# Kernel optimization log

Hardware: AMD Instinct MI355X
Metric: run time of the kernel (lower is better)

The kernel has to match this reference:

```python
import jax, jax.numpy as jnp
import numpy as np

H_SP, W_SP = 8, 8
NUM_HEADS = 6
SHARED = 96
DIM_Q, DIM_KV = 96, 192
WIN = H_SP * W_SP  # 64 tokens per window


def _rel_index():
    # Swin-style relative position index, static numpy computation
    coords = np.stack(np.meshgrid(np.arange(H_SP), np.arange(W_SP), indexing='ij'))
    cf = coords.reshape(2, -1)                      # [2, 64]
    rel = cf[:, :, None] - cf[:, None, :]           # [2, 64, 64]
    rel = rel.transpose(1, 2, 0).astype(np.int64)   # [64, 64, 2]
    rel[..., 0] += H_SP - 1
    rel[..., 1] += W_SP - 1
    rel[..., 0] *= 2 * W_SP - 1
    return rel.sum(-1)                              # [64, 64], values in [0, 225)

REL_IDX = jnp.asarray(_rel_index())


def setup_inputs() -> dict:
    key = jax.random.key(0)
    ks = jax.random.split(key, 12)
    B, H, W = 4, 256, 256
    f32 = jnp.float32
    std = 0.02
    return {
        'x_q':  jax.random.normal(ks[0], (B, DIM_Q, H, W), f32),
        'x_kv': jax.random.normal(ks[1], (B, DIM_KV, H, W), f32),
        'Wq': jax.random.normal(ks[2], (DIM_Q, SHARED), f32) * std,
        'bq': jnp.zeros((SHARED,), f32),
        'Wk': jax.random.normal(ks[3], (DIM_KV, SHARED), f32) * std,
        'bk': jnp.zeros((SHARED,), f32),
        'Wv': jax.random.normal(ks[4], (DIM_KV, SHARED), f32) * std,
        'bv': jnp.zeros((SHARED,), f32),
        'bias_table': jax.random.normal(ks[5], ((2 * H_SP - 1) * (2 * W_SP - 1), NUM_HEADS), f32) * std,
        'Wo': jax.random.normal(ks[6], (SHARED, DIM_Q), f32) * std,
        'bo': jnp.zeros((DIM_Q,), f32),
    }


def reference(x_q, x_kv, Wq, bq, Wk, bk, Wv, bv, bias_table, Wo, bo):
    B, Cq, H, W = x_q.shape
    nH, nW = H // H_SP, W // W_SP  # H, W divisible by window -> pad is a no-op
    hd = SHARED // NUM_HEADS
    scale = hd ** -0.5

    def to_windows(img):
        C = img.shape[1]
        x = img.reshape(B, C, nH, H_SP, nW, W_SP)
        return x.transpose(0, 2, 4, 3, 5, 1).reshape(-1, WIN, C)

    qw = to_windows(x_q)    # [nWin, 64, Cq]
    kvw = to_windows(x_kv)  # [nWin, 64, Ckv]

    def heads(x):
        return x.reshape(-1, WIN, NUM_HEADS, hd).transpose(0, 2, 1, 3)  # [nWin, h, 64, hd]

    q = heads(qw @ Wq + bq)
    k = heads(kvw @ Wk + bk)
    v = heads(kvw @ Wv + bv)

    attn = jnp.einsum('whqd,whkd->whqk', q, k) * scale  # [nWin, h, 64, 64]
    rel_bias = bias_table[REL_IDX].transpose(2, 0, 1)   # [h, 64, 64]
    attn = jax.nn.softmax(attn + rel_bias[None], axis=-1)

    out = jnp.einsum('whqk,whkd->whqd', attn, v)        # [nWin, h, 64, hd]
    out = out.transpose(0, 2, 1, 3).reshape(-1, WIN, SHARED)
    out = out @ Wo + bo                                 # [nWin, 64, Cq]

    # windows2img
    out = out.reshape(B, nH, nW, H_SP, W_SP, Cq)
    out = out.transpose(0, 1, 3, 2, 4, 5).reshape(B, H, W, Cq)
    return out.transpose(0, 3, 1, 2)  # [B, Cq, H, W]
```

## Files before the change

### kernel.cpp

```cpp
#include <hip/hip_runtime.h>

typedef short short8 __attribute__((ext_vector_type(8)));
typedef float f32x4 __attribute__((ext_vector_type(4)));
typedef unsigned short ushort;

#define MFMA(a, b, c) __builtin_amdgcn_mfma_f32_16x16x32_bf16(a, b, c, 0, 0, 0)

#define WS_WQT 0
#define WS_WKT 9216
#define WS_WVT 27648
#define WS_WOT 46080
#define WS_BIAS 55296
#define WS_TOTAL 56646

#define STR_A 104
#define U_A    0
#define U_VT   6656
#define STR_VT 72
#define U_PS   13568
#define U_BIAS 18176
#define U_TOTAL 19526

#define LOG2E 1.44269504f

#define DPP_F(v, ctrl) __int_as_float(__builtin_amdgcn_update_dpp(0, __float_as_int(v), ctrl, 0xF, 0xF, true))

__device__ __forceinline__ ushort f2bf(float x) {
    unsigned u = __float_as_uint(x);
    u = (u + 0x7FFFu + ((u >> 16) & 1u)) >> 16;
    return (ushort)u;
}
__device__ __forceinline__ float bf2f(ushort u) {
    return __uint_as_float(((unsigned)u) << 16);
}

__global__ void prep_weights(const float* __restrict__ Wq, const float* __restrict__ Wk,
                             const float* __restrict__ Wv, const float* __restrict__ Wo,
                             const float* __restrict__ btab, ushort* __restrict__ ws) {
    int idx = blockIdx.x * 256 + threadIdx.x;
    if (idx < WS_WKT) {
        int f = idx >> 9, w = idx & 511, lane = w >> 3, j = w & 7;
        int nt = f / 3, kt = f % 3;
        int n = nt * 16 + (lane & 15), k = kt * 32 + (lane >> 4) * 8 + j;
        ws[idx] = f2bf(Wq[k * 96 + n]);
    } else if (idx < WS_WVT) {
        int t = idx - WS_WKT;
        int f = t >> 9, w = t & 511, lane = w >> 3, j = w & 7;
        int kt6 = f / 6, nt = f % 6;
        int n = nt * 16 + (lane & 15), k = kt6 * 32 + (lane >> 4) * 8 + j;
        ws[idx] = f2bf(Wk[k * 96 + n]);
    } else if (idx < WS_WOT) {
        int t = idx - WS_WVT;
        int f = t >> 9, w = t & 511, lane = w >> 3, j = w & 7;
        int kt6 = f / 6, nt = f % 6;
        int n = nt * 16 + (lane & 15), k = kt6 * 32 + (lane >> 4) * 8 + j;
        ws[idx] = f2bf(Wv[k * 96 + n]);
    } else if (idx < WS_BIAS) {
        int t = idx - WS_WOT;
        int f = t >> 9, w = t & 511, lane = w >> 3, j = w & 7;
        int nt = f / 3, kt = f % 3;
        int n = nt * 16 + (lane & 15), k = kt * 32 + (lane >> 4) * 8 + j;
        ws[idx] = f2bf(Wo[k * 96 + n]);
    } else if (idx < WS_TOTAL) {
        ws[idx] = f2bf(btab[idx - WS_BIAS] * LOG2E);
    }
}

__device__ __forceinline__ void softmax16(f32x4 (&s)[4], float (&pr)[4][4]) {
    #pragma unroll
    for (int r = 0; r < 4; ++r) {
        float m = fmaxf(fmaxf(s[0][r], s[1][r]), fmaxf(s[2][r], s[3][r]));
        m = fmaxf(m, DPP_F(m, 0xB1));
        m = fmaxf(m, DPP_F(m, 0x4E));
        m = fmaxf(m, DPP_F(m, 0x124));
        m = fmaxf(m, DPP_F(m, 0x128));
        float l = 0.f;
        #pragma unroll
        for (int nt = 0; nt < 4; ++nt) { pr[nt][r] = exp2f(s[nt][r] - m); l += pr[nt][r]; }
        l += DPP_F(l, 0xB1); l += DPP_F(l, 0x4E);
        l += DPP_F(l, 0x124); l += DPP_F(l, 0x128);
        float inv = __builtin_amdgcn_rcpf(l);
        #pragma unroll
        for (int nt = 0; nt < 4; ++nt) pr[nt][r] *= inv;
    }
}

__global__ __launch_bounds__(256, 4) void swin_attn(
    const float* __restrict__ xq, const float* __restrict__ xkv,
    const float* __restrict__ bq, const float* __restrict__ bk,
    const float* __restrict__ bv, const float* __restrict__ bo,
    const ushort* __restrict__ ws, float* __restrict__ out)
{
    __shared__ __align__(16) ushort smem[U_TOTAL + 8];
    const int tid = threadIdx.x;
    const int wave = tid >> 6, lane = tid & 63;
    const int l15 = lane & 15, quad = lane >> 4;
    int wid = ((blockIdx.x & 7) << 9) | (blockIdx.x >> 3);
    const int b = wid >> 10;
    const int wh = (wid >> 5) & 31, ww = wid & 31;
    const int h0 = wh * 8, w0 = ww * 8;
    const int mt = wave;

    ushort* A     = smem + U_A;
    ushort* vt    = smem + U_VT;
    ushort* ps    = smem + U_PS + wave * 1152;
    ushort* biasl = smem + U_BIAS;

    float bqr[6], bkr[6], bvr[6];
    #pragma unroll
    for (int h = 0; h < 6; ++h) {
        bqr[h] = bq[h * 16 + l15]; bkr[h] = bk[h * 16 + l15]; bvr[h] = bv[h * 16 + l15];
    }

    int pc[3], pi[3];
    #pragma unroll
    for (int t = 0; t < 3; ++t) { int p = tid + t * 256; pc[t] = p % 96; pi[t] = p / 96; }

    const float* xqb = xq + (size_t)b * 96 * 65536;
    float4 pf[3][2];
    #pragma unroll
    for (int t = 0; t < 3; ++t) {
        const float* g = xqb + (size_t)pc[t] * 65536 + (h0 + pi[t]) * 256 + w0;
        pf[t][0] = *(const float4*)g; pf[t][1] = *(const float4*)(g + 4);
    }
    for (int i = tid; i < 1350; i += 256) biasl[i] = ws[WS_BIAS + i];

    #pragma unroll
    for (int t = 0; t < 3; ++t) {
        int base = (pi[t] * 8) * STR_A + pc[t];
        A[base]             = f2bf(pf[t][0].x); A[base + STR_A]     = f2bf(pf[t][0].y);
        A[base + 2 * STR_A] = f2bf(pf[t][0].z); A[base + 3 * STR_A] = f2bf(pf[t][0].w);
        A[base + 4 * STR_A] = f2bf(pf[t][1].x); A[base + 5 * STR_A] = f2bf(pf[t][1].y);
        A[base + 6 * STR_A] = f2bf(pf[t][1].z); A[base + 7 * STR_A] = f2bf(pf[t][1].w);
    }
    __syncthreads();

    const float* xkvb = xkv + (size_t)b * 192 * 65536;
    float4 pg[3][2];
    #pragma unroll
    for (int t = 0; t < 3; ++t) {
        const float* g = xkvb + (size_t)pc[t] * 65536 + (h0 + pi[t]) * 256 + w0;
        pg[t][0] = *(const float4*)g; pg[t][1] = *(const float4*)(g + 4);
    }

    const int arow = (mt * 16 + l15) * STR_A + quad * 8;
    short8 a0 = *(const short8*)(A + arow);
    short8 a1 = *(const short8*)(A + arow + 32);
    short8 a2 = *(const short8*)(A + arow + 64);
    unsigned qpk[12];
    {
        short8 wq0 = *(const short8*)(ws + WS_WQT + ((0) * 64 + lane) * 8);
        short8 wq1 = *(const short8*)(ws + WS_WQT + ((1) * 64 + lane) * 8);
        short8 wq2 = *(const short8*)(ws + WS_WQT + ((2) * 64 + lane) * 8);
        #pragma unroll
        for (int h = 0; h < 6; ++h) {
            short8 c0 = wq0, c1 = wq1, c2 = wq2;
            if (h < 5) {
                wq0 = *(const short8*)(ws + WS_WQT + (((h + 1) * 3 + 0) * 64 + lane) * 8);
                wq1 = *(const short8*)(ws + WS_WQT + (((h + 1) * 3 + 1) * 64 + lane) * 8);
                wq2 = *(const short8*)(ws + WS_WQT + (((h + 1) * 3 + 2) * 64 + lane) * 8);
            }
            f32x4 qa = {bqr[h], bqr[h], bqr[h], bqr[h]};
            qa = MFMA(a0, c0, qa);
            qa = MFMA(a1, c1, qa);
            qa = MFMA(a2, c2, qa);
            const float qs = 0.25f * LOG2E;
            qpk[h * 2]     = (unsigned)f2bf(qa[0] * qs) | ((unsigned)f2bf(qa[1] * qs) << 16);
            qpk[h * 2 + 1] = (unsigned)f2bf(qa[2] * qs) | ((unsigned)f2bf(qa[3] * qs) << 16);
        }
    }
    __syncthreads();

    #pragma unroll
    for (int t = 0; t < 3; ++t) {
        int base = (pi[t] * 8) * STR_A + pc[t];
        A[base]             = f2bf(pg[t][0].x); A[base + STR_A]     = f2bf(pg[t][0].y);
        A[base + 2 * STR_A] = f2bf(pg[t][0].z); A[base + 3 * STR_A] = f2bf(pg[t][0].w);
        A[base + 4 * STR_A] = f2bf(pg[t][1].x); A[base + 5 * STR_A] = f2bf(pg[t][1].y);
        A[base + 6 * STR_A] = f2bf(pg[t][1].z); A[base + 7 * STR_A] = f2bf(pg[t][1].w);
    }
    __syncthreads();

    f32x4 accK[6], accV[6];
    #pragma unroll
    for (int n = 0; n < 6; ++n) {
        accK[n] = {bkr[n], bkr[n], bkr[n], bkr[n]};
        accV[n] = {bvr[n], bvr[n], bvr[n], bvr[n]};
    }
    #pragma unroll
    for (int kt = 0; kt < 3; ++kt) {
        short8 a = *(const short8*)(A + arow + kt * 32);
        short8 wkf[6], wvf[6];
        #pragma unroll
        for (int nt = 0; nt < 6; ++nt)
            wkf[nt] = *(const short8*)(ws + WS_WKT + (((kt * 6) + nt) * 64 + lane) * 8);
        #pragma unroll
        for (int nt = 0; nt < 6; ++nt)
            wvf[nt] = *(const short8*)(ws + WS_WVT + (((kt * 6) + nt) * 64 + lane) * 8);
        #pragma unroll
        for (int nt = 0; nt < 6; ++nt) accK[nt] = MFMA(a, wkf[nt], accK[nt]);
        #pragma unroll
        for (int nt = 0; nt < 6; ++nt) accV[nt] = MFMA(a, wvf[nt], accV[nt]);
    }
    #pragma unroll
    for (int t = 0; t < 3; ++t) {
        const float* g = xkvb + (size_t)(96 + pc[t]) * 65536 + (h0 + pi[t]) * 256 + w0;
        pf[t][0] = *(const float4*)g; pf[t][1] = *(const float4*)(g + 4);
    }
    __syncthreads();

    #pragma unroll
    for (int t = 0; t < 3; ++t) {
        int base = (pi[t] * 8) * STR_A + pc[t];
        A[base]             = f2bf(pf[t][0].x); A[base + STR_A]     = f2bf(pf[t][0].y);
        A[base + 2 * STR_A] = f2bf(pf[t][0].z); A[base + 3 * STR_A] = f2bf(pf[t][0].w);
        A[base + 4 * STR_A] = f2bf(pf[t][1].x); A[base + 5 * STR_A] = f2bf(pf[t][1].y);
        A[base + 6 * STR_A] = f2bf(pf[t][1].z); A[base + 7 * STR_A] = f2bf(pf[t][1].w);
    }
    __syncthreads();

    #pragma unroll
    for (int kt = 0; kt < 3; ++kt) {
        short8 a = *(const short8*)(A + arow + kt * 32);
        short8 wkf[6], wvf[6];
        #pragma unroll
        for (int nt = 0; nt < 6; ++nt)
            wkf[nt] = *(const short8*)(ws + WS_WKT + ((((3 + kt) * 6) + nt) * 64 + lane) * 8);
        #pragma unroll
        for (int nt = 0; nt < 6; ++nt)
            wvf[nt] = *(const short8*)(ws + WS_WVT + ((((3 + kt) * 6) + nt) * 64 + lane) * 8);
        #pragma unroll
        for (int nt = 0; nt < 6; ++nt) accK[nt] = MFMA(a, wkf[nt], accK[nt]);
        #pragma unroll
        for (int nt = 0; nt < 6; ++nt) accV[nt] = MFMA(a, wvf[nt], accV[nt]);
    }
    #pragma unroll
    for (int nt = 0; nt < 6; ++nt) {
        ushort* dk = A + (mt * 16 + quad * 4) * STR_A + nt * 16 + l15;
        ushort* dv = vt + nt * (16 * STR_VT) + l15 * STR_VT + (mt * 16 + quad * 4);
        #pragma unroll
        for (int r = 0; r < 4; ++r) {
            dk[r * STR_A] = f2bf(accK[nt][r]);
            dv[r]         = f2bf(accV[nt][r]);
        }
    }
    __syncthreads();

    const int qtok0 = mt * 16 + quad * 4;
    unsigned bidxp[4][2];
    #pragma unroll
    for (int nt = 0; nt < 4; ++nt) {
        int kt2 = nt * 16 + l15, i2 = kt2 >> 3, j2 = kt2 & 7;
        unsigned v[4];
        #pragma unroll
        for (int r = 0; r < 4; ++r) {
            int qt = qtok0 + r, i1 = qt >> 3, j1 = qt & 7;
            v[r] = (unsigned)(((i1 - i2 + 7) * 15 + (j1 - j2 + 7)) * 6);
        }
        bidxp[nt][0] = v[0] | (v[1] << 16);
        bidxp[nt][1] = v[2] | (v[3] << 16);
    }

    f32x4 accO[6];
    short8 zero8 = {};
    #pragma unroll
    for (int hp = 0; hp < 3; ++hp) {
        const int hA = hp * 2, hB = hA + 1;
        asm volatile("" ::: "memory");
        unsigned wloA = qpk[hA * 2], whiA = qpk[hA * 2 + 1];
        unsigned wloB = qpk[hB * 2], whiB = qpk[hB * 2 + 1];
        ps[(quad * 4 + 0) * 24 + l15] = (ushort)wloA;
        ps[(quad * 4 + 1) * 24 + l15] = (ushort)(wloA >> 16);
        ps[(quad * 4 + 2) * 24 + l15] = (ushort)whiA;
        ps[(quad * 4 + 3) * 24 + l15] = (ushort)(whiA >> 16);
        ps[384 + (quad * 4 + 0) * 24 + l15] = (ushort)wloB;
        ps[384 + (quad * 4 + 1) * 24 + l15] = (ushort)(wloB >> 16);
        ps[384 + (quad * 4 + 2) * 24 + l15] = (ushort)whiB;
        ps[384 + (quad * 4 + 3) * 24 + l15] = (ushort)(whiB >> 16);
        short8 aqA = zero8, aqB = zero8;
        short8 kfA[4] = {zero8, zero8, zero8, zero8};
        short8 kfB[4] = {zero8, zero8, zero8, zero8};
        if (quad < 2) {
            aqA = *(const short8*)(ps + l15 * 24 + quad * 8);
            aqB = *(const short8*)(ps + 384 + l15 * 24 + quad * 8);
            #pragma unroll
            for (int nt = 0; nt < 4; ++nt) {
                kfA[nt] = *(const short8*)(A + (nt * 16 + l15) * STR_A + hA * 16 + quad * 8);
                kfB[nt] = *(const short8*)(A + (nt * 16 + l15) * STR_A + hB * 16 + quad * 8);
            }
        }
        f32x4 sA[4], sB[4];
        #pragma unroll
        for (int nt = 0; nt < 4; ++nt) {
            unsigned i01 = bidxp[nt][0], i23 = bidxp[nt][1];
            f32x4 c;
            c[0] = bf2f(biasl[(i01 & 0xFFFFu) + hA]); c[1] = bf2f(biasl[(i01 >> 16) + hA]);
            c[2] = bf2f(biasl[(i23 & 0xFFFFu) + hA]); c[3] = bf2f(biasl[(i23 >> 16) + hA]);
            sA[nt] = MFMA(aqA, kfA[nt], c);
        }
        #pragma unroll
        for (int nt = 0; nt < 4; ++nt) {
            unsigned i01 = bidxp[nt][0], i23 = bidxp[nt][1];
            f32x4 c;
            c[0] = bf2f(biasl[(i01 & 0xFFFFu) + hB]); c[1] = bf2f(biasl[(i01 >> 16) + hB]);
            c[2] = bf2f(biasl[(i23 & 0xFFFFu) + hB]); c[3] = bf2f(biasl[(i23 >> 16) + hB]);
            sB[nt] = MFMA(aqB, kfB[nt], c);
        }
        float prA[4][4], prB[4][4];
        softmax16(sA, prA);
        softmax16(sB, prB);
        asm volatile("" ::: "memory");
        #pragma unroll
        for (int nt = 0; nt < 4; ++nt)
            #pragma unroll
            for (int r = 0; r < 4; ++r)
                ps[(quad * 4 + r) * 72 + nt * 16 + l15] = f2bf(prA[nt][r]);
        f32x4 oA = {};
        #pragma unroll
        for (int k2 = 0; k2 < 2; ++k2) {
            short8 ap  = *(const short8*)(ps + l15 * 72 + k2 * 32 + quad * 8);
            short8 bv8 = *(const short8*)(vt + hA * (16 * STR_VT) + l15 * STR_VT + k2 * 32 + quad * 8);
            oA = MFMA(ap, bv8, oA);
        }
        asm volatile("" ::: "memory");
        #pragma unroll
        for (int nt = 0; nt < 4; ++nt)
            #pragma unroll
            for (int r = 0; r < 4; ++r)
                ps[(quad * 4 + r) * 72 + nt * 16 + l15] = f2bf(prB[nt][r]);
        f32x4 oB = {};
        #pragma unroll
        for (int k2 = 0; k2 < 2; ++k2) {
            short8 ap  = *(const short8*)(ps + l15 * 72 + k2 * 32 + quad * 8);
            short8 bv8 = *(const short8*)(vt + hB * (16 * STR_VT) + l15 * STR_VT + k2 * 32 + quad * 8);
            oB = MFMA(ap, bv8, oB);
        }
        accO[hA] = oA; accO[hB] = oB;
    }
    __syncthreads();

    float bor_[6];
    #pragma unroll
    for (int h = 0; h < 6; ++h) bor_[h] = bo[h * 16 + l15];
    ushort* obuf = A;
    #pragma unroll
    for (int h = 0; h < 6; ++h)
        #pragma unroll
        for (int r = 0; r < 4; ++r)
            obuf[(mt * 16 + quad * 4 + r) * STR_A + h * 16 + l15] = f2bf(accO[h][r]);

    {
        int t0 = mt * 16 + quad * 4;
        int i = t0 >> 3, j0 = t0 & 7;
        short8 oa0 = *(const short8*)(obuf + arow);
        short8 oa1 = *(const short8*)(obuf + arow + 32);
        short8 oa2 = *(const short8*)(obuf + arow + 64);
        short8 wo0 = *(const short8*)(ws + WS_WOT + ((0) * 64 + lane) * 8);
        short8 wo1 = *(const short8*)(ws + WS_WOT + ((1) * 64 + lane) * 8);
        short8 wo2 = *(const short8*)(ws + WS_WOT + ((2) * 64 + lane) * 8);
        #pragma unroll
        for (int nt = 0; nt < 6; ++nt) {
            short8 c0 = wo0, c1 = wo1, c2 = wo2;
            if (nt < 5) {
                wo0 = *(const short8*)(ws + WS_WOT + (((nt + 1) * 3 + 0) * 64 + lane) * 8);
                wo1 = *(const short8*)(ws + WS_WOT + (((nt + 1) * 3 + 1) * 64 + lane) * 8);
                wo2 = *(const short8*)(ws + WS_WOT + (((nt + 1) * 3 + 2) * 64 + lane) * 8);
            }
            f32x4 acc = {bor_[nt], bor_[nt], bor_[nt], bor_[nt]};
            acc = MFMA(oa0, c0, acc);
            acc = MFMA(oa1, c1, acc);
            acc = MFMA(oa2, c2, acc);
            int cout = nt * 16 + l15;
            float4 v4 = make_float4(acc[0], acc[1], acc[2], acc[3]);
            float* dst = out + (size_t)(b * 96 + cout) * 65536 + (h0 + i) * 256 + w0 + j0;
            *(float4*)dst = v4;
        }
    }
}

extern "C" void kernel_launch(void* const* d_in, const int* in_sizes, int n_in,
                              void* d_out, int out_size, void* d_ws, size_t ws_size,
                              hipStream_t stream) {
    const float* xq   = (const float*)d_in[0];
    const float* xkv  = (const float*)d_in[1];
    const float* Wq   = (const float*)d_in[2];
    const float* bq   = (const float*)d_in[3];
    const float* Wk   = (const float*)d_in[4];
    const float* bk   = (const float*)d_in[5];
    const float* Wv   = (const float*)d_in[6];
    const float* bv   = (const float*)d_in[7];
    const float* btab = (const float*)d_in[8];
    const float* Wo   = (const float*)d_in[9];
    const float* bo   = (const float*)d_in[10];
    ushort* ws = (ushort*)d_ws;
    float* out = (float*)d_out;

    hipLaunchKernelGGL(prep_weights, dim3((WS_TOTAL + 255) / 256), dim3(256), 0, stream,
                       Wq, Wk, Wv, Wo, btab, ws);
    hipLaunchKernelGGL(swin_attn, dim3(4096), dim3(256), 0, stream,
                       xq, xkv, bq, bk, bv, bo, ws, out);
}
```

Before: 485.7 us.

## Transpose QK^T mapping, use bpermute for Q, prefetch K/V weights, pack bf16

Swaps MFMA operand order for the Q projection and QK^T so each lane holds a full key column per query, which turns softmax reductions into two cross-lane shuffles instead of DPP chains. Q fragments move between lanes with ds_bpermute instead of a shared-memory round trip. K/V weight fragments are software-prefetched one k-step ahead, with asm pins to force early issue. Conversions use v_cvt_pk_bf16_f32, and head-pair bias values are read with one 32-bit load. Occupancy hint drops from 4 to 3 waves per SIMD to make room for the extra live registers.

```diff
diff --git a/kernel.cpp b/kernel.cpp
--- a/kernel.cpp
+++ b/kernel.cpp
@@ -2,9 +2,15 @@
 
 typedef short short8 __attribute__((ext_vector_type(8)));
 typedef float f32x4 __attribute__((ext_vector_type(4)));
+typedef int int4v __attribute__((ext_vector_type(4)));
+typedef unsigned uint2v __attribute__((ext_vector_type(2)));
 typedef unsigned short ushort;
 
 #define MFMA(a, b, c) __builtin_amdgcn_mfma_f32_16x16x32_bf16(a, b, c, 0, 0, 0)
+
+#define PIN8(v8_) do { int4v _t; __builtin_memcpy(&_t, &(v8_), 16); \
+    asm volatile("" :: "v"(_t[0]), "v"(_t[1]), "v"(_t[2]), "v"(_t[3])); } while (0)
+#define PINF4(v4_) asm volatile("" :: "v"((v4_).x), "v"((v4_).y), "v"((v4_).z), "v"((v4_).w))
 
 #define WS_WQT 0
 #define WS_WKT 9216
@@ -23,15 +29,15 @@
 
 #define LOG2E 1.44269504f
 
-#define DPP_F(v, ctrl) __int_as_float(__builtin_amdgcn_update_dpp(0, __float_as_int(v), ctrl, 0xF, 0xF, true))
-
-__device__ __forceinline__ ushort f2bf(float x) {
-    unsigned u = __float_as_uint(x);
+__device__ __forceinline__ ushort f2bf(float v) {
+    unsigned u = __float_as_uint(v);
     u = (u + 0x7FFFu + ((u >> 16) & 1u)) >> 16;
     return (ushort)u;
 }
-__device__ __forceinline__ float bf2f(ushort u) {
-    return __uint_as_float(((unsigned)u) << 16);
+__device__ __forceinline__ unsigned cvtpk_bf16(float lo, float hi) {
+    unsigned r;
+    asm("v_cvt_pk_bf16_f32 %0, %1, %2" : "=v"(r) : "v"(lo), "v"(hi));
+    return r;
 }
 
 __global__ void prep_weights(const float* __restrict__ Wq, const float* __restrict__ Wk,
@@ -66,26 +72,7 @@
     }
 }
 
-__device__ __forceinline__ void softmax16(f32x4 (&s)[4], float (&pr)[4][4]) {
-    #pragma unroll
-    for (int r = 0; r < 4; ++r) {
-        float m = fmaxf(fmaxf(s[0][r], s[1][r]), fmaxf(s[2][r], s[3][r]));
-        m = fmaxf(m, DPP_F(m, 0xB1));
-        m = fmaxf(m, DPP_F(m, 0x4E));
-        m = fmaxf(m, DPP_F(m, 0x124));
-        m = fmaxf(m, DPP_F(m, 0x128));
-        float l = 0.f;
-        #pragma unroll
-        for (int nt = 0; nt < 4; ++nt) { pr[nt][r] = exp2f(s[nt][r] - m); l += pr[nt][r]; }
-        l += DPP_F(l, 0xB1); l += DPP_F(l, 0x4E);
-        l += DPP_F(l, 0x124); l += DPP_F(l, 0x128);
-        float inv = __builtin_amdgcn_rcpf(l);
-        #pragma unroll
-        for (int nt = 0; nt < 4; ++nt) pr[nt][r] *= inv;
-    }
-}
-
-__global__ __launch_bounds__(256, 4) void swin_attn(
+__global__ __launch_bounds__(256, 3) void swin_attn(
     const float* __restrict__ xq, const float* __restrict__ xkv,
     const float* __restrict__ bq, const float* __restrict__ bk,
     const float* __restrict__ bv, const float* __restrict__ bo,
@@ -106,11 +93,9 @@
     ushort* ps    = smem + U_PS + wave * 1152;
     ushort* biasl = smem + U_BIAS;
 
-    float bqr[6], bkr[6], bvr[6];
-    #pragma unroll
-    for (int h = 0; h < 6; ++h) {
-        bqr[h] = bq[h * 16 + l15]; bkr[h] = bk[h * 16 + l15]; bvr[h] = bv[h * 16 + l15];
-    }
+    float bkr[6], bvr[6];
+    #pragma unroll
+    for (int h = 0; h < 6; ++h) { bkr[h] = bk[h * 16 + l15]; bvr[h] = bv[h * 16 + l15]; }
 
     int pc[3], pi[3];
     #pragma unroll
@@ -141,7 +126,11 @@
     for (int t = 0; t < 3; ++t) {
         const float* g = xkvb + (size_t)pc[t] * 65536 + (h0 + pi[t]) * 256 + w0;
         pg[t][0] = *(const float4*)g; pg[t][1] = *(const float4*)(g + 4);
-    }
+        PINF4(pg[t][0]); PINF4(pg[t][1]);
+    }
+    float4 bqv[6];
+    #pragma unroll
+    for (int h = 0; h < 6; ++h) { bqv[h] = *(const float4*)(bq + h * 16 + quad * 4); PINF4(bqv[h]); }
 
     const int arow = (mt * 16 + l15) * STR_A + quad * 8;
     short8 a0 = *(const short8*)(A + arow);
@@ -149,9 +138,10 @@
     short8 a2 = *(const short8*)(A + arow + 64);
     unsigned qpk[12];
     {
-        short8 wq0 = *(const short8*)(ws + WS_WQT + ((0) * 64 + lane) * 8);
-        short8 wq1 = *(const short8*)(ws + WS_WQT + ((1) * 64 + lane) * 8);
-        short8 wq2 = *(const short8*)(ws + WS_WQT + ((2) * 64 + lane) * 8);
+        short8 wq0 = *(const short8*)(ws + WS_WQT + (0 * 64 + lane) * 8);
+        short8 wq1 = *(const short8*)(ws + WS_WQT + (1 * 64 + lane) * 8);
+        short8 wq2 = *(const short8*)(ws + WS_WQT + (2 * 64 + lane) * 8);
+        PIN8(wq0); PIN8(wq1); PIN8(wq2);
         #pragma unroll
         for (int h = 0; h < 6; ++h) {
             short8 c0 = wq0, c1 = wq1, c2 = wq2;
@@ -159,14 +149,15 @@
                 wq0 = *(const short8*)(ws + WS_WQT + (((h + 1) * 3 + 0) * 64 + lane) * 8);
                 wq1 = *(const short8*)(ws + WS_WQT + (((h + 1) * 3 + 1) * 64 + lane) * 8);
                 wq2 = *(const short8*)(ws + WS_WQT + (((h + 1) * 3 + 2) * 64 + lane) * 8);
-            }
-            f32x4 qa = {bqr[h], bqr[h], bqr[h], bqr[h]};
-            qa = MFMA(a0, c0, qa);
-            qa = MFMA(a1, c1, qa);
-            qa = MFMA(a2, c2, qa);
+                PIN8(wq0); PIN8(wq1); PIN8(wq2);
+            }
+            f32x4 qa = {bqv[h].x, bqv[h].y, bqv[h].z, bqv[h].w};
+            qa = MFMA(c0, a0, qa);
+            qa = MFMA(c1, a1, qa);
+            qa = MFMA(c2, a2, qa);
             const float qs = 0.25f * LOG2E;
-            qpk[h * 2]     = (unsigned)f2bf(qa[0] * qs) | ((unsigned)f2bf(qa[1] * qs) << 16);
-            qpk[h * 2 + 1] = (unsigned)f2bf(qa[2] * qs) | ((unsigned)f2bf(qa[3] * qs) << 16);
+            qpk[h * 2]     = cvtpk_bf16(qa[0] * qs, qa[1] * qs);
+            qpk[h * 2 + 1] = cvtpk_bf16(qa[2] * qs, qa[3] * qs);
         }
     }
     __syncthreads();
@@ -179,33 +170,50 @@
         A[base + 4 * STR_A] = f2bf(pg[t][1].x); A[base + 5 * STR_A] = f2bf(pg[t][1].y);
         A[base + 6 * STR_A] = f2bf(pg[t][1].z); A[base + 7 * STR_A] = f2bf(pg[t][1].w);
     }
-    __syncthreads();
-
     f32x4 accK[6], accV[6];
     #pragma unroll
     for (int n = 0; n < 6; ++n) {
         accK[n] = {bkr[n], bkr[n], bkr[n], bkr[n]};
         accV[n] = {bvr[n], bvr[n], bvr[n], bvr[n]};
     }
+    short8 wk[6], wv[6];
+    #pragma unroll
+    for (int nt = 0; nt < 6; ++nt) {
+        wk[nt] = *(const short8*)(ws + WS_WKT + (nt * 64 + lane) * 8); PIN8(wk[nt]);
+    }
+    #pragma unroll
+    for (int nt = 0; nt < 6; ++nt) {
+        wv[nt] = *(const short8*)(ws + WS_WVT + (nt * 64 + lane) * 8); PIN8(wv[nt]);
+    }
+    __syncthreads();
+
     #pragma unroll
     for (int kt = 0; kt < 3; ++kt) {
         short8 a = *(const short8*)(A + arow + kt * 32);
-        short8 wkf[6], wvf[6];
-        #pragma unroll
-        for (int nt = 0; nt < 6; ++nt)
-            wkf[nt] = *(const short8*)(ws + WS_WKT + (((kt * 6) + nt) * 64 + lane) * 8);
-        #pragma unroll
-        for (int nt = 0; nt < 6; ++nt)
-            wvf[nt] = *(const short8*)(ws + WS_WVT + (((kt * 6) + nt) * 64 + lane) * 8);
-        #pragma unroll
-        for (int nt = 0; nt < 6; ++nt) accK[nt] = MFMA(a, wkf[nt], accK[nt]);
-        #pragma unroll
-        for (int nt = 0; nt < 6; ++nt) accV[nt] = MFMA(a, wvf[nt], accV[nt]);
+        #pragma unroll
+        for (int nt = 0; nt < 6; ++nt) accK[nt] = MFMA(a, wk[nt], accK[nt]);
+        if (kt < 2) {
+            #pragma unroll
+            for (int nt = 0; nt < 6; ++nt) {
+                wk[nt] = *(const short8*)(ws + WS_WKT + ((((kt + 1) * 6) + nt) * 64 + lane) * 8);
+                PIN8(wk[nt]);
+            }
+        }
+        #pragma unroll
+        for (int nt = 0; nt < 6; ++nt) accV[nt] = MFMA(a, wv[nt], accV[nt]);
+        if (kt < 2) {
+            #pragma unroll
+            for (int nt = 0; nt < 6; ++nt) {
+                wv[nt] = *(const short8*)(ws + WS_WVT + ((((kt + 1) * 6) + nt) * 64 + lane) * 8);
+                PIN8(wv[nt]);
+            }
+        }
     }
     #pragma unroll
     for (int t = 0; t < 3; ++t) {
         const float* g = xkvb + (size_t)(96 + pc[t]) * 65536 + (h0 + pi[t]) * 256 + w0;
         pf[t][0] = *(const float4*)g; pf[t][1] = *(const float4*)(g + 4);
+        PINF4(pf[t][0]); PINF4(pf[t][1]);
     }
     __syncthreads();
 
@@ -217,22 +225,37 @@
         A[base + 4 * STR_A] = f2bf(pf[t][1].x); A[base + 5 * STR_A] = f2bf(pf[t][1].y);
         A[base + 6 * STR_A] = f2bf(pf[t][1].z); A[base + 7 * STR_A] = f2bf(pf[t][1].w);
     }
+    #pragma unroll
+    for (int nt = 0; nt < 6; ++nt) {
+        wk[nt] = *(const short8*)(ws + WS_WKT + (((3 * 6) + nt) * 64 + lane) * 8); PIN8(wk[nt]);
+    }
+    #pragma unroll
+    for (int nt = 0; nt < 6; ++nt) {
+        wv[nt] = *(const short8*)(ws + WS_WVT + (((3 * 6) + nt) * 64 + lane) * 8); PIN8(wv[nt]);
+    }
     __syncthreads();
 
     #pragma unroll
     for (int kt = 0; kt < 3; ++kt) {
         short8 a = *(const short8*)(A + arow + kt * 32);
-        short8 wkf[6], wvf[6];
-        #pragma unroll
-        for (int nt = 0; nt < 6; ++nt)
-            wkf[nt] = *(const short8*)(ws + WS_WKT + ((((3 + kt) * 6) + nt) * 64 + lane) * 8);
-        #pragma unroll
-        for (int nt = 0; nt < 6; ++nt)
-            wvf[nt] = *(const short8*)(ws + WS_WVT + ((((3 + kt) * 6) + nt) * 64 + lane) * 8);
-        #pragma unroll
-        for (int nt = 0; nt < 6; ++nt) accK[nt] = MFMA(a, wkf[nt], accK[nt]);
-        #pragma unroll
-        for (int nt = 0; nt < 6; ++nt) accV[nt] = MFMA(a, wvf[nt], accV[nt]);
+        #pragma unroll
+        for (int nt = 0; nt < 6; ++nt) accK[nt] = MFMA(a, wk[nt], accK[nt]);
+        if (kt < 2) {
+            #pragma unroll
+            for (int nt = 0; nt < 6; ++nt) {
+                wk[nt] = *(const short8*)(ws + WS_WKT + ((((4 + kt) * 6) + nt) * 64 + lane) * 8);
+                PIN8(wk[nt]);
+            }
+        }
+        #pragma unroll
+        for (int nt = 0; nt < 6; ++nt) accV[nt] = MFMA(a, wv[nt], accV[nt]);
+        if (kt < 2) {
+            #pragma unroll
+            for (int nt = 0; nt < 6; ++nt) {
+                wv[nt] = *(const short8*)(ws + WS_WVT + ((((4 + kt) * 6) + nt) * 64 + lane) * 8);
+                PIN8(wv[nt]);
+            }
+        }
     }
     #pragma unroll
     for (int nt = 0; nt < 6; ++nt) {
@@ -246,92 +269,133 @@
     }
     __syncthreads();
 
-    const int qtok0 = mt * 16 + quad * 4;
-    unsigned bidxp[4][2];
-    #pragma unroll
-    for (int nt = 0; nt < 4; ++nt) {
-        int kt2 = nt * 16 + l15, i2 = kt2 >> 3, j2 = kt2 & 7;
-        unsigned v[4];
+    const int qt = mt * 16 + l15;
+    const int i1 = qt >> 3, j1 = qt & 7;
+    int boff[4][4];
+    #pragma unroll
+    for (int nt = 0; nt < 4; ++nt)
         #pragma unroll
         for (int r = 0; r < 4; ++r) {
-            int qt = qtok0 + r, i1 = qt >> 3, j1 = qt & 7;
-            v[r] = (unsigned)(((i1 - i2 + 7) * 15 + (j1 - j2 + 7)) * 6);
-        }
-        bidxp[nt][0] = v[0] | (v[1] << 16);
-        bidxp[nt][1] = v[2] | (v[3] << 16);
-    }
+            int k2 = nt * 16 + quad * 4 + r, i2 = k2 >> 3, j2 = k2 & 7;
+            boff[nt][r] = ((i1 - i2 + 7) * 15 + (j1 - j2 + 7)) * 6;
+        }
+
+    const int bp0 = (l15 + (quad << 5)) << 2;
+    const int bp1 = bp0 + (16 << 2);
+    const int psrow = l15 * 72;
 
     f32x4 accO[6];
     short8 zero8 = {};
     #pragma unroll
     for (int hp = 0; hp < 3; ++hp) {
         const int hA = hp * 2, hB = hA + 1;
-        asm volatile("" ::: "memory");
-        unsigned wloA = qpk[hA * 2], whiA = qpk[hA * 2 + 1];
-        unsigned wloB = qpk[hB * 2], whiB = qpk[hB * 2 + 1];
-        ps[(quad * 4 + 0) * 24 + l15] = (ushort)wloA;
-        ps[(quad * 4 + 1) * 24 + l15] = (ushort)(wloA >> 16);
-        ps[(quad * 4 + 2) * 24 + l15] = (ushort)whiA;
-        ps[(quad * 4 + 3) * 24 + l15] = (ushort)(whiA >> 16);
-        ps[384 + (quad * 4 + 0) * 24 + l15] = (ushort)wloB;
-        ps[384 + (quad * 4 + 1) * 24 + l15] = (ushort)(wloB >> 16);
-        ps[384 + (quad * 4 + 2) * 24 + l15] = (ushort)whiB;
-        ps[384 + (quad * 4 + 3) * 24 + l15] = (ushort)(whiB >> 16);
-        short8 aqA = zero8, aqB = zero8;
-        short8 kfA[4] = {zero8, zero8, zero8, zero8};
-        short8 kfB[4] = {zero8, zero8, zero8, zero8};
+        int A0 = __builtin_amdgcn_ds_bpermute(bp0, (int)qpk[hA * 2]);
+        int A1 = __builtin_amdgcn_ds_bpermute(bp0, (int)qpk[hA * 2 + 1]);
+        int A2 = __builtin_amdgcn_ds_bpermute(bp1, (int)qpk[hA * 2]);
+        int A3 = __builtin_amdgcn_ds_bpermute(bp1, (int)qpk[hA * 2 + 1]);
+        int B0 = __builtin_amdgcn_ds_bpermute(bp0, (int)qpk[hB * 2]);
+        int B1 = __builtin_amdgcn_ds_bpermute(bp0, (int)qpk[hB * 2 + 1]);
+        int B2 = __builtin_amdgcn_ds_bpermute(bp1, (int)qpk[hB * 2]);
+        int B3 = __builtin_amdgcn_ds_bpermute(bp1, (int)qpk[hB * 2 + 1]);
+        union { int4v i; short8 s; } ua, ub;
+        ua.i = (int4v){A0, A1, A2, A3};
+        ub.i = (int4v){B0, B1, B2, B3};
+        short8 aqA = ua.s, aqB = ub.s;
+
+        short8 kfA[4], kfB[4];
+        #pragma unroll
+        for (int nt = 0; nt < 4; ++nt) { kfA[nt] = zero8; kfB[nt] = zero8; }
         if (quad < 2) {
-            aqA = *(const short8*)(ps + l15 * 24 + quad * 8);
-            aqB = *(const short8*)(ps + 384 + l15 * 24 + quad * 8);
             #pragma unroll
             for (int nt = 0; nt < 4; ++nt) {
                 kfA[nt] = *(const short8*)(A + (nt * 16 + l15) * STR_A + hA * 16 + quad * 8);
                 kfB[nt] = *(const short8*)(A + (nt * 16 + l15) * STR_A + hB * 16 + quad * 8);
             }
         }
+        unsigned bb[4][4];
+        #pragma unroll
+        for (int nt = 0; nt < 4; ++nt)
+            #pragma unroll
+            for (int r = 0; r < 4; ++r)
+                bb[nt][r] = *(const unsigned*)(biasl + boff[nt][r] + hA);
+
         f32x4 sA[4], sB[4];
         #pragma unroll
         for (int nt = 0; nt < 4; ++nt) {
-            unsigned i01 = bidxp[nt][0], i23 = bidxp[nt][1];
             f32x4 c;
-            c[0] = bf2f(biasl[(i01 & 0xFFFFu) + hA]); c[1] = bf2f(biasl[(i01 >> 16) + hA]);
-            c[2] = bf2f(biasl[(i23 & 0xFFFFu) + hA]); c[3] = bf2f(biasl[(i23 >> 16) + hA]);
-            sA[nt] = MFMA(aqA, kfA[nt], c);
+            c[0] = __uint_as_float(bb[nt][0] << 16); c[1] = __uint_as_float(bb[nt][1] << 16);
+            c[2] = __uint_as_float(bb[nt][2] << 16); c[3] = __uint_as_float(bb[nt][3] << 16);
+            sA[nt] = MFMA(kfA[nt], aqA, c);
         }
         #pragma unroll
         for (int nt = 0; nt < 4; ++nt) {
-            unsigned i01 = bidxp[nt][0], i23 = bidxp[nt][1];
             f32x4 c;
-            c[0] = bf2f(biasl[(i01 & 0xFFFFu) + hB]); c[1] = bf2f(biasl[(i01 >> 16) + hB]);
-            c[2] = bf2f(biasl[(i23 & 0xFFFFu) + hB]); c[3] = bf2f(biasl[(i23 >> 16) + hB]);
-            sB[nt] = MFMA(aqB, kfB[nt], c);
-        }
-        float prA[4][4], prB[4][4];
-        softmax16(sA, prA);
-        softmax16(sB, prB);
-        asm volatile("" ::: "memory");
+            c[0] = __uint_as_float(bb[nt][0] & 0xFFFF0000u); c[1] = __uint_as_float(bb[nt][1] & 0xFFFF0000u);
+            c[2] = __uint_as_float(bb[nt][2] & 0xFFFF0000u); c[3] = __uint_as_float(bb[nt][3] & 0xFFFF0000u);
+            sB[nt] = MFMA(kfB[nt], aqB, c);
+        }
+        float mA, mB, lA, lB;
+        {
+            float a_ = fmaxf(fmaxf(sA[0][0], sA[0][1]), fmaxf(sA[0][2], sA[0][3]));
+            float b_ = fmaxf(fmaxf(sA[1][0], sA[1][1]), fmaxf(sA[1][2], sA[1][3]));
+            float c_ = fmaxf(fmaxf(sA[2][0], sA[2][1]), fmaxf(sA[2][2], sA[2][3]));
+            float d_ = fmaxf(fmaxf(sA[3][0], sA[3][1]), fmaxf(sA[3][2], sA[3][3]));
+            mA = fmaxf(fmaxf(a_, b_), fmaxf(c_, d_));
+            float a2_ = fmaxf(fmaxf(sB[0][0], sB[0][1]), fmaxf(sB[0][2], sB[0][3]));
+            float b2_ = fmaxf(fmaxf(sB[1][0], sB[1][1]), fmaxf(sB[1][2], sB[1][3]));
+            float c2_ = fmaxf(fmaxf(sB[2][0], sB[2][1]), fmaxf(sB[2][2], sB[2][3]));
+            float d2_ = fmaxf(fmaxf(sB[3][0], sB[3][1]), fmaxf(sB[3][2], sB[3][3]));
+            mB = fmaxf(fmaxf(a2_, b2_), fmaxf(c2_, d2_));
+        }
+        mA = fmaxf(mA, __shfl_xor(mA, 16)); mA = fmaxf(mA, __shfl_xor(mA, 32));
+        mB = fmaxf(mB, __shfl_xor(mB, 16)); mB = fmaxf(mB, __shfl_xor(mB, 32));
         #pragma unroll
         for (int nt = 0; nt < 4; ++nt)
             #pragma unroll
-            for (int r = 0; r < 4; ++r)
-                ps[(quad * 4 + r) * 72 + nt * 16 + l15] = f2bf(prA[nt][r]);
+            for (int r = 0; r < 4; ++r) {
+                sA[nt][r] = exp2f(sA[nt][r] - mA);
+                sB[nt][r] = exp2f(sB[nt][r] - mB);
+            }
+        {
+            float a_ = (sA[0][0] + sA[0][1]) + (sA[0][2] + sA[0][3]);
+            float b_ = (sA[1][0] + sA[1][1]) + (sA[1][2] + sA[1][3]);
+            float c_ = (sA[2][0] + sA[2][1]) + (sA[2][2] + sA[2][3]);
+            float d_ = (sA[3][0] + sA[3][1]) + (sA[3][2] + sA[3][3]);
+            lA = (a_ + b_) + (c_ + d_);
+            float a2_ = (sB[0][0] + sB[0][1]) + (sB[0][2] + sB[0][3]);
+            float b2_ = (sB[1][0] + sB[1][1]) + (sB[1][2] + sB[1][3]);
+            float c2_ = (sB[2][0] + sB[2][1]) + (sB[2][2] + sB[2][3]);
+            float d2_ = (sB[3][0] + sB[3][1]) + (sB[3][2] + sB[3][3]);
+            lB = (a2_ + b2_) + (c2_ + d2_);
+        }
+        lA += __shfl_xor(lA, 16); lA += __shfl_xor(lA, 32);
+        lB += __shfl_xor(lB, 16); lB += __shfl_xor(lB, 32);
+        float invA = __builtin_amdgcn_rcpf(lA);
+        float invB = __builtin_amdgcn_rcpf(lB);
+
+        #pragma unroll
+        for (int nt = 0; nt < 4; ++nt) {
+            unsigned p0 = cvtpk_bf16(sA[nt][0] * invA, sA[nt][1] * invA);
+            unsigned p1 = cvtpk_bf16(sA[nt][2] * invA, sA[nt][3] * invA);
+            *(uint2v*)(ps + psrow + nt * 16 + quad * 4) = (uint2v){p0, p1};
+        }
         f32x4 oA = {};
         #pragma unroll
         for (int k2 = 0; k2 < 2; ++k2) {
-            short8 ap  = *(const short8*)(ps + l15 * 72 + k2 * 32 + quad * 8);
+            short8 ap  = *(const short8*)(ps + psrow + k2 * 32 + quad * 8);
             short8 bv8 = *(const short8*)(vt + hA * (16 * STR_VT) + l15 * STR_VT + k2 * 32 + quad * 8);
             oA = MFMA(ap, bv8, oA);
         }
-        asm volatile("" ::: "memory");
-        #pragma unroll
-        for (int nt = 0; nt < 4; ++nt)
-            #pragma unroll
-            for (int r = 0; r < 4; ++r)
-                ps[(quad * 4 + r) * 72 + nt * 16 + l15] = f2bf(prB[nt][r]);
+        #pragma unroll
+        for (int nt = 0; nt < 4; ++nt) {
+            unsigned p0 = cvtpk_bf16(sB[nt][0] * invB, sB[nt][1] * invB);
+            unsigned p1 = cvtpk_bf16(sB[nt][2] * invB, sB[nt][3] * invB);
+            *(uint2v*)(ps + psrow + nt * 16 + quad * 4) = (uint2v){p0, p1};
+        }
         f32x4 oB = {};
         #pragma unroll
         for (int k2 = 0; k2 < 2; ++k2) {
-            short8 ap  = *(const short8*)(ps + l15 * 72 + k2 * 32 + quad * 8);
+            short8 ap  = *(const short8*)(ps + psrow + k2 * 32 + quad * 8);
             short8 bv8 = *(const short8*)(vt + hB * (16 * STR_VT) + l15 * STR_VT + k2 * 32 + quad * 8);
             oB = MFMA(ap, bv8, oB);
         }
@@ -355,9 +419,10 @@
         short8 oa0 = *(const short8*)(obuf + arow);
         short8 oa1 = *(const short8*)(obuf + arow + 32);
         short8 oa2 = *(const short8*)(obuf + arow + 64);
-        short8 wo0 = *(const short8*)(ws + WS_WOT + ((0) * 64 + lane) * 8);
-        short8 wo1 = *(const short8*)(ws + WS_WOT + ((1) * 64 + lane) * 8);
-        short8 wo2 = *(const short8*)(ws + WS_WOT + ((2) * 64 + lane) * 8);
+        short8 wo0 = *(const short8*)(ws + WS_WOT + (0 * 64 + lane) * 8);
+        short8 wo1 = *(const short8*)(ws + WS_WOT + (1 * 64 + lane) * 8);
+        short8 wo2 = *(const short8*)(ws + WS_WOT + (2 * 64 + lane) * 8);
+        PIN8(wo0); PIN8(wo1); PIN8(wo2);
         #pragma unroll
         for (int nt = 0; nt < 6; ++nt) {
             short8 c0 = wo0, c1 = wo1, c2 = wo2;
@@ -365,6 +430,7 @@
                 wo0 = *(const short8*)(ws + WS_WOT + (((nt + 1) * 3 + 0) * 64 + lane) * 8);
                 wo1 = *(const short8*)(ws + WS_WOT + (((nt + 1) * 3 + 1) * 64 + lane) * 8);
                 wo2 = *(const short8*)(ws + WS_WOT + (((nt + 1) * 3 + 2) * 64 + lane) * 8);
+                PIN8(wo0); PIN8(wo1); PIN8(wo2);
             }
             f32x4 acc = {bor_[nt], bor_[nt], bor_[nt], bor_[nt]};
             acc = MFMA(oa0, c0, acc);
```

After: 554.4 us. 1.14x slower.

## Remap input staging per token, pack bf16 conversions, defer softmax normalization

Applied to the files above, without the earlier changes.

Each lane now loads one token across 24 channels, so the input tile is written to LDS as packed bf16 vectors with `v_cvt_pk_bf16_f32`. This replaces many scattered 16-bit stores. The first K/V input chunk is staged in the V-transpose region, which removes one barrier between the Q projection and the K/V projection. Softmax no longer subtracts the row max, and normalization moves after the PV MFMA as a per-row scale. Bias values for the two heads are fetched with a single 32-bit LDS load. Dropping the max subtraction risks overflow in exp2 if scores grow large, and the new global loads are 4-byte scalars instead of float4.

```diff
diff --git a/kernel.cpp b/kernel.cpp
--- a/kernel.cpp
+++ b/kernel.cpp
@@ -2,9 +2,11 @@
 
 typedef short short8 __attribute__((ext_vector_type(8)));
 typedef float f32x4 __attribute__((ext_vector_type(4)));
+typedef unsigned uint4v __attribute__((ext_vector_type(4)));
 typedef unsigned short ushort;
 
 #define MFMA(a, b, c) __builtin_amdgcn_mfma_f32_16x16x32_bf16(a, b, c, 0, 0, 0)
+#define DPP_F(v, ctrl) __int_as_float(__builtin_amdgcn_update_dpp(0, __float_as_int(v), ctrl, 0xF, 0xF, true))
 
 #define WS_WQT 0
 #define WS_WKT 9216
@@ -23,15 +25,15 @@
 
 #define LOG2E 1.44269504f
 
-#define DPP_F(v, ctrl) __int_as_float(__builtin_amdgcn_update_dpp(0, __float_as_int(v), ctrl, 0xF, 0xF, true))
-
-__device__ __forceinline__ ushort f2bf(float x) {
-    unsigned u = __float_as_uint(x);
+__device__ __forceinline__ ushort f2bf(float v) {
+    unsigned u = __float_as_uint(v);
     u = (u + 0x7FFFu + ((u >> 16) & 1u)) >> 16;
     return (ushort)u;
 }
-__device__ __forceinline__ float bf2f(ushort u) {
-    return __uint_as_float(((unsigned)u) << 16);
+__device__ __forceinline__ unsigned cvtpk_bf16(float lo, float hi) {
+    unsigned r;
+    asm("v_cvt_pk_bf16_f32 %0, %1, %2" : "=v"(r) : "v"(lo), "v"(hi));
+    return r;
 }
 
 __global__ void prep_weights(const float* __restrict__ Wq, const float* __restrict__ Wk,
@@ -66,25 +68,6 @@
     }
 }
 
-__device__ __forceinline__ void softmax16(f32x4 (&s)[4], float (&pr)[4][4]) {
-    #pragma unroll
-    for (int r = 0; r < 4; ++r) {
-        float m = fmaxf(fmaxf(s[0][r], s[1][r]), fmaxf(s[2][r], s[3][r]));
-        m = fmaxf(m, DPP_F(m, 0xB1));
-        m = fmaxf(m, DPP_F(m, 0x4E));
-        m = fmaxf(m, DPP_F(m, 0x124));
-        m = fmaxf(m, DPP_F(m, 0x128));
-        float l = 0.f;
-        #pragma unroll
-        for (int nt = 0; nt < 4; ++nt) { pr[nt][r] = exp2f(s[nt][r] - m); l += pr[nt][r]; }
-        l += DPP_F(l, 0xB1); l += DPP_F(l, 0x4E);
-        l += DPP_F(l, 0x124); l += DPP_F(l, 0x128);
-        float inv = __builtin_amdgcn_rcpf(l);
-        #pragma unroll
-        for (int nt = 0; nt < 4; ++nt) pr[nt][r] *= inv;
-    }
-}
-
 __global__ __launch_bounds__(256, 4) void swin_attn(
     const float* __restrict__ xq, const float* __restrict__ xkv,
     const float* __restrict__ bq, const float* __restrict__ bk,
@@ -102,7 +85,7 @@
     const int mt = wave;
 
     ushort* A     = smem + U_A;
-    ushort* vt    = smem + U_VT;
+    ushort* vtreg = smem + U_VT;
     ushort* ps    = smem + U_PS + wave * 1152;
     ushort* biasl = smem + U_BIAS;
 
@@ -112,72 +95,65 @@
         bqr[h] = bq[h * 16 + l15]; bkr[h] = bk[h * 16 + l15]; bvr[h] = bv[h * 16 + l15];
     }
 
-    int pc[3], pi[3];
-    #pragma unroll
-    for (int t = 0; t < 3; ++t) { int p = tid + t * 256; pc[t] = p % 96; pi[t] = p / 96; }
+    const int c0   = __builtin_amdgcn_readfirstlane(wave * 24);
+    const int toff = (h0 + (lane >> 3)) * 256 + w0 + (lane & 7);
+    const int wdst = lane * STR_A + c0;
+    const int arow = (mt * 16 + l15) * STR_A + quad * 8;
 
     const float* xqb = xq + (size_t)b * 96 * 65536;
-    float4 pf[3][2];
-    #pragma unroll
-    for (int t = 0; t < 3; ++t) {
-        const float* g = xqb + (size_t)pc[t] * 65536 + (h0 + pi[t]) * 256 + w0;
-        pf[t][0] = *(const float4*)g; pf[t][1] = *(const float4*)(g + 4);
-    }
+    float vq[24];
+    #pragma unroll
+    for (int j = 0; j < 24; ++j) vq[j] = xqb[(size_t)(c0 + j) * 65536 + toff];
     for (int i = tid; i < 1350; i += 256) biasl[i] = ws[WS_BIAS + i];
-
-    #pragma unroll
-    for (int t = 0; t < 3; ++t) {
-        int base = (pi[t] * 8) * STR_A + pc[t];
-        A[base]             = f2bf(pf[t][0].x); A[base + STR_A]     = f2bf(pf[t][0].y);
-        A[base + 2 * STR_A] = f2bf(pf[t][0].z); A[base + 3 * STR_A] = f2bf(pf[t][0].w);
-        A[base + 4 * STR_A] = f2bf(pf[t][1].x); A[base + 5 * STR_A] = f2bf(pf[t][1].y);
-        A[base + 6 * STR_A] = f2bf(pf[t][1].z); A[base + 7 * STR_A] = f2bf(pf[t][1].w);
+    {
+        unsigned u[12];
+        #pragma unroll
+        for (int j = 0; j < 12; ++j) u[j] = cvtpk_bf16(vq[2 * j], vq[2 * j + 1]);
+        uint4v* d = (uint4v*)(A + wdst);
+        d[0] = (uint4v){u[0], u[1], u[2], u[3]};
+        d[1] = (uint4v){u[4], u[5], u[6], u[7]};
+        d[2] = (uint4v){u[8], u[9], u[10], u[11]};
     }
     __syncthreads();
 
     const float* xkvb = xkv + (size_t)b * 192 * 65536;
-    float4 pg[3][2];
-    #pragma unroll
-    for (int t = 0; t < 3; ++t) {
-        const float* g = xkvb + (size_t)pc[t] * 65536 + (h0 + pi[t]) * 256 + w0;
-        pg[t][0] = *(const float4*)g; pg[t][1] = *(const float4*)(g + 4);
-    }
-
-    const int arow = (mt * 16 + l15) * STR_A + quad * 8;
+    float vk0[24];
+    #pragma unroll
+    for (int j = 0; j < 24; ++j) vk0[j] = xkvb[(size_t)(c0 + j) * 65536 + toff];
+
     short8 a0 = *(const short8*)(A + arow);
     short8 a1 = *(const short8*)(A + arow + 32);
     short8 a2 = *(const short8*)(A + arow + 64);
     unsigned qpk[12];
     {
-        short8 wq0 = *(const short8*)(ws + WS_WQT + ((0) * 64 + lane) * 8);
-        short8 wq1 = *(const short8*)(ws + WS_WQT + ((1) * 64 + lane) * 8);
-        short8 wq2 = *(const short8*)(ws + WS_WQT + ((2) * 64 + lane) * 8);
+        short8 wq0 = *(const short8*)(ws + WS_WQT + (0 * 64 + lane) * 8);
+        short8 wq1 = *(const short8*)(ws + WS_WQT + (1 * 64 + lane) * 8);
+        short8 wq2 = *(const short8*)(ws + WS_WQT + (2 * 64 + lane) * 8);
         #pragma unroll
         for (int h = 0; h < 6; ++h) {
-            short8 c0 = wq0, c1 = wq1, c2 = wq2;
+            short8 c0f = wq0, c1f = wq1, c2f = wq2;
             if (h < 5) {
                 wq0 = *(const short8*)(ws + WS_WQT + (((h + 1) * 3 + 0) * 64 + lane) * 8);
                 wq1 = *(const short8*)(ws + WS_WQT + (((h + 1) * 3 + 1) * 64 + lane) * 8);
                 wq2 = *(const short8*)(ws + WS_WQT + (((h + 1) * 3 + 2) * 64 + lane) * 8);
             }
             f32x4 qa = {bqr[h], bqr[h], bqr[h], bqr[h]};
-            qa = MFMA(a0, c0, qa);
-            qa = MFMA(a1, c1, qa);
-            qa = MFMA(a2, c2, qa);
+            qa = MFMA(a0, c0f, qa);
+            qa = MFMA(a1, c1f, qa);
+            qa = MFMA(a2, c2f, qa);
             const float qs = 0.25f * LOG2E;
-            qpk[h * 2]     = (unsigned)f2bf(qa[0] * qs) | ((unsigned)f2bf(qa[1] * qs) << 16);
-            qpk[h * 2 + 1] = (unsigned)f2bf(qa[2] * qs) | ((unsigned)f2bf(qa[3] * qs) << 16);
-        }
-    }
-    __syncthreads();
-
-    #pragma unroll
-    for (int t = 0; t < 3; ++t) {
-        int base = (pi[t] * 8) * STR_A + pc[t];
-        A[base]             = f2bf(pg[t][0].x); A[base + STR_A]     = f2bf(pg[t][0].y);
-        A[base + 2 * STR_A] = f2bf(pg[t][0].z); A[base + 3 * STR_A] = f2bf(pg[t][0].w);
-        A[base + 4 * STR_A] = f2bf(pg[t][1].x); A[base + 5 * STR_A] = f2bf(pg[t][1].y);
-        A[base + 6 * STR_A] = f2bf(pg[t][1].z); A[base + 7 * STR_A] = f2bf(pg[t][1].w);
+            qpk[h * 2]     = cvtpk_bf16(qa[0] * qs, qa[1] * qs);
+            qpk[h * 2 + 1] = cvtpk_bf16(qa[2] * qs, qa[3] * qs);
+        }
+    }
+    {
+        unsigned u[12];
+        #pragma unroll
+        for (int j = 0; j < 12; ++j) u[j] = cvtpk_bf16(vk0[2 * j], vk0[2 * j + 1]);
+        uint4v* d = (uint4v*)(vtreg + wdst);
+        d[0] = (uint4v){u[0], u[1], u[2], u[3]};
+        d[1] = (uint4v){u[4], u[5], u[6], u[7]};
+        d[2] = (uint4v){u[8], u[9], u[10], u[11]};
     }
     __syncthreads();
 
@@ -189,7 +165,7 @@
     }
     #pragma unroll
     for (int kt = 0; kt < 3; ++kt) {
-        short8 a = *(const short8*)(A + arow + kt * 32);
+        short8 a = *(const short8*)(vtreg + arow + kt * 32);
         short8 wkf[6], wvf[6];
         #pragma unroll
         for (int nt = 0; nt < 6; ++nt)
@@ -202,20 +178,17 @@
         #pragma unroll
         for (int nt = 0; nt < 6; ++nt) accV[nt] = MFMA(a, wvf[nt], accV[nt]);
     }
-    #pragma unroll
-    for (int t = 0; t < 3; ++t) {
-        const float* g = xkvb + (size_t)(96 + pc[t]) * 65536 + (h0 + pi[t]) * 256 + w0;
-        pf[t][0] = *(const float4*)g; pf[t][1] = *(const float4*)(g + 4);
-    }
-    __syncthreads();
-
-    #pragma unroll
-    for (int t = 0; t < 3; ++t) {
-        int base = (pi[t] * 8) * STR_A + pc[t];
-        A[base]             = f2bf(pf[t][0].x); A[base + STR_A]     = f2bf(pf[t][0].y);
-        A[base + 2 * STR_A] = f2bf(pf[t][0].z); A[base + 3 * STR_A] = f2bf(pf[t][0].w);
-        A[base + 4 * STR_A] = f2bf(pf[t][1].x); A[base + 5 * STR_A] = f2bf(pf[t][1].y);
-        A[base + 6 * STR_A] = f2bf(pf[t][1].z); A[base + 7 * STR_A] = f2bf(pf[t][1].w);
+    {
+        float vk1[24];
+        #pragma unroll
+        for (int j = 0; j < 24; ++j) vk1[j] = xkvb[(size_t)(96 + c0 + j) * 65536 + toff];
+        unsigned u[12];
+        #pragma unroll
+        for (int j = 0; j < 12; ++j) u[j] = cvtpk_bf16(vk1[2 * j], vk1[2 * j + 1]);
+        uint4v* d = (uint4v*)(A + wdst);
+        d[0] = (uint4v){u[0], u[1], u[2], u[3]};
+        d[1] = (uint4v){u[4], u[5], u[6], u[7]};
+        d[2] = (uint4v){u[8], u[9], u[10], u[11]};
     }
     __syncthreads();
 
@@ -237,7 +210,7 @@
     #pragma unroll
     for (int nt = 0; nt < 6; ++nt) {
         ushort* dk = A + (mt * 16 + quad * 4) * STR_A + nt * 16 + l15;
-        ushort* dv = vt + nt * (16 * STR_VT) + l15 * STR_VT + (mt * 16 + quad * 4);
+        ushort* dv = vtreg + nt * (16 * STR_VT) + l15 * STR_VT + (mt * 16 + quad * 4);
         #pragma unroll
         for (int r = 0; r < 4; ++r) {
             dk[r * STR_A] = f2bf(accK[nt][r]);
@@ -289,26 +262,46 @@
                 kfB[nt] = *(const short8*)(A + (nt * 16 + l15) * STR_A + hB * 16 + quad * 8);
             }
         }
-        f32x4 sA[4], sB[4];
+        unsigned bb[4][4];
         #pragma unroll
         for (int nt = 0; nt < 4; ++nt) {
             unsigned i01 = bidxp[nt][0], i23 = bidxp[nt][1];
+            bb[nt][0] = *(const unsigned*)(biasl + (i01 & 0xFFFFu) + hA);
+            bb[nt][1] = *(const unsigned*)(biasl + (i01 >> 16) + hA);
+            bb[nt][2] = *(const unsigned*)(biasl + (i23 & 0xFFFFu) + hA);
+            bb[nt][3] = *(const unsigned*)(biasl + (i23 >> 16) + hA);
+        }
+        f32x4 sA[4], sB[4];
+        #pragma unroll
+        for (int nt = 0; nt < 4; ++nt) {
             f32x4 c;
-            c[0] = bf2f(biasl[(i01 & 0xFFFFu) + hA]); c[1] = bf2f(biasl[(i01 >> 16) + hA]);
-            c[2] = bf2f(biasl[(i23 & 0xFFFFu) + hA]); c[3] = bf2f(biasl[(i23 >> 16) + hA]);
+            c[0] = __uint_as_float(bb[nt][0] << 16); c[1] = __uint_as_float(bb[nt][1] << 16);
+            c[2] = __uint_as_float(bb[nt][2] << 16); c[3] = __uint_as_float(bb[nt][3] << 16);
             sA[nt] = MFMA(aqA, kfA[nt], c);
         }
         #pragma unroll
         for (int nt = 0; nt < 4; ++nt) {
-            unsigned i01 = bidxp[nt][0], i23 = bidxp[nt][1];
             f32x4 c;
-            c[0] = bf2f(biasl[(i01 & 0xFFFFu) + hB]); c[1] = bf2f(biasl[(i01 >> 16) + hB]);
-            c[2] = bf2f(biasl[(i23 & 0xFFFFu) + hB]); c[3] = bf2f(biasl[(i23 >> 16) + hB]);
+            c[0] = __uint_as_float(bb[nt][0] & 0xFFFF0000u); c[1] = __uint_as_float(bb[nt][1] & 0xFFFF0000u);
+            c[2] = __uint_as_float(bb[nt][2] & 0xFFFF0000u); c[3] = __uint_as_float(bb[nt][3] & 0xFFFF0000u);
             sB[nt] = MFMA(aqB, kfB[nt], c);
         }
-        float prA[4][4], prB[4][4];
-        softmax16(sA, prA);
-        softmax16(sB, prB);
+        float prA[4][4], prB[4][4], invA4[4], invB4[4];
+        #pragma unroll
+        for (int r = 0; r < 4; ++r) {
+            float lA = 0.f, lB = 0.f;
+            #pragma unroll
+            for (int nt = 0; nt < 4; ++nt) {
+                prA[nt][r] = exp2f(sA[nt][r]); lA += prA[nt][r];
+                prB[nt][r] = exp2f(sB[nt][r]); lB += prB[nt][r];
+            }
+            lA += DPP_F(lA, 0xB1);  lB += DPP_F(lB, 0xB1);
+            lA += DPP_F(lA, 0x4E);  lB += DPP_F(lB, 0x4E);
+            lA += DPP_F(lA, 0x124); lB += DPP_F(lB, 0x124);
+            lA += DPP_F(lA, 0x128); lB += DPP_F(lB, 0x128);
+            invA4[r] = __builtin_amdgcn_rcpf(lA);
+            invB4[r] = __builtin_amdgcn_rcpf(lB);
+        }
         asm volatile("" ::: "memory");
         #pragma unroll
         for (int nt = 0; nt < 4; ++nt)
@@ -319,9 +312,11 @@
         #pragma unroll
         for (int k2 = 0; k2 < 2; ++k2) {
             short8 ap  = *(const short8*)(ps + l15 * 72 + k2 * 32 + quad * 8);
-            short8 bv8 = *(const short8*)(vt + hA * (16 * STR_VT) + l15 * STR_VT + k2 * 32 + quad * 8);
+            short8 bv8 = *(const short8*)(vtreg + hA * (16 * STR_VT) + l15 * STR_VT + k2 * 32 + quad * 8);
             oA = MFMA(ap, bv8, oA);
         }
+        #pragma unroll
+        for (int r = 0; r < 4; ++r) oA[r] *= invA4[r];
         asm volatile("" ::: "memory");
         #pragma unroll
         for (int nt = 0; nt < 4; ++nt)
@@ -332,9 +327,11 @@
         #pragma unroll
         for (int k2 = 0; k2 < 2; ++k2) {
             short8 ap  = *(const short8*)(ps + l15 * 72 + k2 * 32 + quad * 8);
-            short8 bv8 = *(const short8*)(vt + hB * (16 * STR_VT) + l15 * STR_VT + k2 * 32 + quad * 8);
+            short8 bv8 = *(const short8*)(vtreg + hB * (16 * STR_VT) + l15 * STR_VT + k2 * 32 + quad * 8);
             oB = MFMA(ap, bv8, oB);
         }
+        #pragma unroll
+        for (int r = 0; r < 4; ++r) oB[r] *= invB4[r];
         accO[hA] = oA; accO[hB] = oB;
     }
     __syncthreads();
@@ -355,21 +352,21 @@
         short8 oa0 = *(const short8*)(obuf + arow);
         short8 oa1 = *(const short8*)(obuf + arow + 32);
         short8 oa2 = *(const short8*)(obuf + arow + 64);
-        short8 wo0 = *(const short8*)(ws + WS_WOT + ((0) * 64 + lane) * 8);
-        short8 wo1 = *(const short8*)(ws + WS_WOT + ((1) * 64 + lane) * 8);
-        short8 wo2 = *(const short8*)(ws + WS_WOT + ((2) * 64 + lane) * 8);
+        short8 wo0 = *(const short8*)(ws + WS_WOT + (0 * 64 + lane) * 8);
+        short8 wo1 = *(const short8*)(ws + WS_WOT + (1 * 64 + lane) * 8);
+        short8 wo2 = *(const short8*)(ws + WS_WOT + (2 * 64 + lane) * 8);
         #pragma unroll
         for (int nt = 0; nt < 6; ++nt) {
-            short8 c0 = wo0, c1 = wo1, c2 = wo2;
+            short8 c0f = wo0, c1f = wo1, c2f = wo2;
             if (nt < 5) {
                 wo0 = *(const short8*)(ws + WS_WOT + (((nt + 1) * 3 + 0) * 64 + lane) * 8);
                 wo1 = *(const short8*)(ws + WS_WOT + (((nt + 1) * 3 + 1) * 64 + lane) * 8);
                 wo2 = *(const short8*)(ws + WS_WOT + (((nt + 1) * 3 + 2) * 64 + lane) * 8);
             }
             f32x4 acc = {bor_[nt], bor_[nt], bor_[nt], bor_[nt]};
-            acc = MFMA(oa0, c0, acc);
-            acc = MFMA(oa1, c1, acc);
-            acc = MFMA(oa2, c2, acc);
+            acc = MFMA(oa0, c0f, acc);
+            acc = MFMA(oa1, c1f, acc);
+            acc = MFMA(oa2, c2f, acc);
             int cout = nt * 16 + l15;
             float4 v4 = make_float4(acc[0], acc[1], acc[2], acc[3]);
             float* dst = out + (size_t)(b * 96 + cout) * 65536 + (h0 + i) * 256 + w0 + j0;
```

New measurement: 463.7 us. 4.5% less time.
